# Kernel tuning notes

Hardware: AMD Instinct MI355X
Metric: run time of the kernel (lower is better)

## Reference

```python
import jax, jax.numpy as jnp
import numpy as np

LOW_THRESH, HIGH_THRESH = 0.1, 0.2   # kornia canny defaults
HYST_ITERS = 10                      # fixed-point hysteresis iterations (fixed for jit)


def _gaussian_kernel5(sigma=1.0):
    x = jnp.arange(5, dtype=jnp.float32) - 2.0
    g = jnp.exp(-0.5 * (x / sigma) ** 2)
    g = g / g.sum()
    return jnp.outer(g, g)  # [5,5]


def _conv2d(x, k):
    # x: [B,1,H,W]; k: [kh,kw]; reflect pad + VALID conv == SAME with reflect border
    kh, kw = k.shape
    xp = jnp.pad(x, ((0, 0), (0, 0), (kh // 2, kh // 2), (kw // 2, kw // 2)), mode="reflect")
    return jax.lax.conv_general_dilated(
        xp, k[None, None], (1, 1), "VALID",
        dimension_numbers=("NCHW", "OIHW", "NCHW"))


def _shift(x, dy, dx):
    # value of neighbor at (i+dy, j+dx), zero-padded border; x: [B,1,H,W]
    H, W = x.shape[2], x.shape[3]
    xp = jnp.pad(x, ((0, 0), (0, 0), (1, 1), (1, 1)))
    return xp[:, :, 1 + dy:1 + dy + H, 1 + dx:1 + dx + W]


def _canny_edges(img):
    # img: [B,3,H,W] in [0,1] -> binary edge map [B,1,H,W]
    gray = 0.299 * img[:, :1] + 0.587 * img[:, 1:2] + 0.114 * img[:, 2:3]
    blur = _conv2d(gray, _gaussian_kernel5())
    sobel_x = jnp.array([[-1., 0., 1.], [-2., 0., 2.], [-1., 0., 1.]], jnp.float32)
    gx = _conv2d(blur, sobel_x)
    gy = _conv2d(blur, sobel_x.T)
    mag = jnp.sqrt(gx * gx + gy * gy + 1e-12)
    ang = jnp.arctan2(gy, gx)

    # non-maximum suppression: quantize gradient direction to 4 bins (0/45/90/135 deg)
    b = jnp.mod(jnp.round(ang / (jnp.pi / 4.0)), 4).astype(jnp.int32)  # [B,1,H,W]
    n_pos = jnp.stack([_shift(mag, 0, 1), _shift(mag, 1, 1),
                       _shift(mag, 1, 0), _shift(mag, 1, -1)], axis=0)  # [4,B,1,H,W]
    n_neg = jnp.stack([_shift(mag, 0, -1), _shift(mag, -1, -1),
                       _shift(mag, -1, 0), _shift(mag, -1, 1)], axis=0)
    n1 = jnp.take_along_axis(n_pos, b[None], axis=0)[0]
    n2 = jnp.take_along_axis(n_neg, b[None], axis=0)[0]
    nms = jnp.where((mag >= n1) & (mag >= n2), mag, 0.0)

    # double threshold: strong=1.0, weak=0.5
    edges = jnp.where(nms >= HIGH_THRESH, 1.0,
                      jnp.where(nms >= LOW_THRESH, 0.5, 0.0))

    # hysteresis: weak pixels with a strong 8-neighbor become strong (iterated)
    def body(_, e):
        strong = (e == 1.0).astype(e.dtype)
        nb = jax.lax.reduce_window(strong, 0.0, jax.lax.max,
                                   (1, 1, 3, 3), (1, 1, 1, 1), "SAME")
        promoted = (e == 0.5) & (nb > 0.5)
        return jnp.where(promoted, 1.0, e)

    edges = jax.lax.fori_loop(0, HYST_ITERS, body, edges)
    return (edges == 1.0).astype(jnp.float32)


def setup_inputs() -> dict:
    key = jax.random.key(0)
    k1, k2 = jax.random.split(key)
    shape = (16, 3, 512, 512)
    return {"y_hat": jax.random.uniform(k1, shape, jnp.float32),
            "y": jax.random.uniform(k2, shape, jnp.float32)}


def reference(y_hat, y):
    y_hat_edges = _canny_edges(y_hat)
    y_edges = _canny_edges(y)
    return jnp.mean(jnp.abs(y_hat_edges - y_edges))  # F.l1_loss, mean reduction
```

## Files before the change

kernel.cpp:

```cpp
#include <hip/hip_runtime.h>
#include <math.h>

#define H 512
#define W 512
#define IMG (H*W)
#define NIMG 32

typedef unsigned long long u64;

__device__ __forceinline__ int reflect_idx(int i, int n) {
    if (i < 0) i = -i;
    if (i >= n) i = 2 * n - 2 - i;
    return i;
}

#define S0 0.05448868454964294f
#define S1 0.35317871110251920f
#define S2 0.94551131545035710f
#define S3 1.29364257779496160f
#define A1 0.05448868454964294f
#define A2 0.24420134200323332f
#define A3 0.34813126234460456f

#define TY 32

__global__ __launch_bounds__(512) void k_edges(const float* __restrict__ yhat,
                                               const float* __restrict__ yy,
                                               u64* __restrict__ strongP,
                                               u64* __restrict__ weakP) {
    __shared__ __align__(16) char lds[12768 + 22848];
    float (*sg)[76] = (float (*)[76])lds;
    float (*hxy)[68][2] = (float (*)[68][2])(lds + 12768);
    float (*sm)[68] = (float (*)[68])lds;
    unsigned char (*sbin)[68] = (unsigned char (*)[68])(lds + 9792);

    const int n = blockIdx.z;
    const float* src = (n < 16) ? (yhat + (size_t)n * 3 * IMG)
                                : (yy + (size_t)(n - 16) * 3 * IMG);
    const int x0 = blockIdx.x * 64;
    const int y0 = blockIdx.y * TY;
    const int tx = threadIdx.x, ty = threadIdx.y;
    const int tid = ty * 64 + tx;

    const int ixA = reflect_idx(x0 - 4 + tx, W);
    const int ixB = reflect_idx(x0 + 60 + tx, W);
#pragma unroll
    for (int k = 0; k < 6; k++) {
        int sy = ty + 8 * k;
        if (sy < 42) {
            int iy = reflect_idx(y0 - 4 + sy, H);
            const float* row = src + iy * W;
            float r = row[ixA], g = row[IMG + ixA], b = row[2 * IMG + ixA];
            sg[sy][tx] = 0.299f * r + 0.587f * g + 0.114f * b;
            if (tx < 8) {
                float r2 = row[ixB], g2 = row[IMG + ixB], b2 = row[2 * IMG + ixB];
                sg[sy][64 + tx] = 0.299f * r2 + 0.587f * g2 + 0.114f * b2;
            }
        }
    }
    __syncthreads();

    for (int t = tid; t < 714; t += 512) {
        int sy = t / 17, g = t % 17;
        const float4* p = (const float4*)&sg[sy][0];
        float4 q0 = p[g], q1 = p[g + 1], q2 = p[g + 2];
        float w[12] = {q0.x, q0.y, q0.z, q0.w, q1.x, q1.y, q1.z, q1.w,
                       q2.x, q2.y, q2.z, q2.w};
#pragma unroll
        for (int j = 0; j < 4; j++) {
            float hx = A3 * (w[j + 4] - w[j + 2]) + A2 * (w[j + 5] - w[j + 1])
                     + A1 * (w[j + 6] - w[j + 0]);
            float hy = S3 * w[j + 3] + S2 * (w[j + 4] + w[j + 2])
                     + S1 * (w[j + 5] + w[j + 1]) + S0 * (w[j + 6] + w[j + 0]);
            *(float2*)&hxy[sy][4 * g + j][0] = make_float2(hx, hy);
        }
    }
    __syncthreads();

    for (int t = tid; t < 594; t += 512) {
        int rg = t / 66, c = t % 66;
        float hx[10], hy[10];
#pragma unroll
        for (int i = 0; i < 10; i++) {
            float2 v = *(const float2*)&hxy[4 * rg + i][c][0];
            hx[i] = v.x; hy[i] = v.y;
        }
        int imgcol = x0 - 1 + c;
        bool colok = (unsigned)imgcol < (unsigned)W;
#pragma unroll
        for (int j = 0; j < 4; j++) {
            int my = 4 * rg + j;
            float gx = S3 * hx[j + 3] + S2 * (hx[j + 4] + hx[j + 2])
                     + S1 * (hx[j + 5] + hx[j + 1]) + S0 * (hx[j + 6] + hx[j + 0]);
            float gy = A3 * (hy[j + 4] - hy[j + 2]) + A2 * (hy[j + 5] - hy[j + 1])
                     + A1 * (hy[j + 6] - hy[j + 0]);
            int imgrow = y0 - 1 + my;
            bool ok = colok && ((unsigned)imgrow < (unsigned)H);
            float m = ok ? sqrtf(gx * gx + gy * gy + 1e-12f) : 0.f;
            sm[my][c] = m;
            float ax = fabsf(gx), ay = fabsf(gy);
            int d;
            if (ay <= 0.4142135623730951f * ax) d = 1;
            else if (ay >= 2.414213562373095f * ax) d = 68;
            else d = ((gx > 0.f) == (gy > 0.f)) ? 69 : 67;
            sbin[my][c] = (unsigned char)d;
        }
    }
    __syncthreads();

#pragma unroll
    for (int k = 0; k < 4; k++) {
        int ry = ty + 8 * k;
        const float* cp = &sm[ry + 1][tx + 1];
        float mag = cp[0];
        int d = sbin[ry + 1][tx + 1];
        float n1 = cp[d];
        float n2 = cp[-d];
        float nms = (mag >= n1 && mag >= n2) ? mag : 0.f;
        u64 strong = __ballot(nms >= 0.2f);
        u64 weak = __ballot(nms >= 0.1f);
        if (tx == 0) {
            size_t off = ((size_t)n * H + (y0 + ry)) * 8 + blockIdx.x;
            strongP[off] = strong;
            weakP[off] = weak;
        }
    }
}

__device__ __forceinline__ u64 ldw(const u64* p, int img, int y, int w, bool ok) {
    return (ok && w >= 0 && w < 8) ? p[((size_t)img * H + y) * 8 + w] : 0ULL;
}

__global__ __launch_bounds__(256) void k_hyst(const u64* __restrict__ strongP,
                                              const u64* __restrict__ weakP,
                                              unsigned int* __restrict__ partials) {
    __shared__ unsigned int part[4];
    const int wy = threadIdx.x >> 6;
    const int wave = blockIdx.x * 4 + wy;
    const int lane = threadIdx.x & 63;
    const int tile = wave & 255;
    const int pair = wave >> 8;
    const int tx0 = (tile & 15) * 32;
    const int ty0 = (tile >> 4) * 32;

    const int y = ty0 - 10 + lane;
    const bool rowok = (lane < 52) && (y >= 0) && (y < H);
    const int s = tx0 - 10;
    const int w0i = s >> 6;
    const int r = s & 63;

    const int imgA = pair, imgB = pair + 16;
    u64 sA, wA, sB, wB;
    {
        u64 lo, hi;
        lo = ldw(strongP, imgA, y, w0i, rowok); hi = ldw(strongP, imgA, y, w0i + 1, rowok);
        sA = (lo >> r) | (hi << (64 - r));
        lo = ldw(weakP, imgA, y, w0i, rowok);   hi = ldw(weakP, imgA, y, w0i + 1, rowok);
        wA = (lo >> r) | (hi << (64 - r));
        lo = ldw(strongP, imgB, y, w0i, rowok); hi = ldw(strongP, imgB, y, w0i + 1, rowok);
        sB = (lo >> r) | (hi << (64 - r));
        lo = ldw(weakP, imgB, y, w0i, rowok);   hi = ldw(weakP, imgB, y, w0i + 1, rowok);
        wB = (lo >> r) | (hi << (64 - r));
    }

#pragma unroll
    for (int it = 0; it < 10; it++) {
        u64 up = __shfl_up(sA, 1), dn = __shfl_down(sA, 1);
        u64 t = up | sA | dn;
        sA |= (t | (t << 1) | (t >> 1)) & wA;
        up = __shfl_up(sB, 1); dn = __shfl_down(sB, 1);
        t = up | sB | dn;
        sB |= (t | (t << 1) | (t >> 1)) & wB;
    }

    unsigned int c = 0;
    if (lane >= 10 && lane < 42) {
        const u64 mask = ((1ULL << 42) - (1ULL << 10));
        c = (unsigned int)__popcll((sA ^ sB) & mask);
    }
#pragma unroll
    for (int off = 32; off > 0; off >>= 1) c += __shfl_down(c, off);
    if (lane == 0) part[wy] = c;
    __syncthreads();
    if (threadIdx.x == 0)
        partials[blockIdx.x] = part[0] + part[1] + part[2] + part[3];
}

__global__ __launch_bounds__(256) void k_final(const unsigned int* __restrict__ partials,
                                               float* __restrict__ out) {
    __shared__ unsigned int part[4];
    unsigned int c = 0;
    for (int i = threadIdx.x; i < 1024; i += 256) c += partials[i];
#pragma unroll
    for (int off = 32; off > 0; off >>= 1) c += __shfl_down(c, off);
    const int lane = threadIdx.x & 63;
    const int wy = threadIdx.x >> 6;
    if (lane == 0) part[wy] = c;
    __syncthreads();
    if (threadIdx.x == 0)
        out[0] = (float)(part[0] + part[1] + part[2] + part[3]) * (1.0f / 4194304.0f);
}

extern "C" void kernel_launch(void* const* d_in, const int* in_sizes, int n_in,
                              void* d_out, int out_size, void* d_ws, size_t ws_size,
                              hipStream_t stream) {
    const float* yhat = (const float*)d_in[0];
    const float* yy = (const float*)d_in[1];

    u64* strongP = (u64*)d_ws;
    u64* weakP = strongP + (size_t)NIMG * H * 8;
    unsigned int* partials = (unsigned int*)(weakP + (size_t)NIMG * H * 8);

    dim3 eblk(64, 8);
    dim3 egrd(W / 64, H / TY, NIMG);
    k_edges<<<egrd, eblk, 0, stream>>>(yhat, yy, strongP, weakP);

    k_hyst<<<1024, 256, 0, stream>>>(strongP, weakP, partials);
    k_final<<<1, 256, 0, stream>>>(partials, (float*)d_out);
}
```

Before: 155.9 us.

## Vectorize gray tile loads with float4 and transpose bitplane layout for coalesced reads

Interior tiles now load the RGB halo with aligned float4 reads over an 80-wide shared-memory row that starts at x0-8. Border tiles fall back to a scalar reflect path. The strong and weak bitplanes are stored column-word-major (image, word, row), so the hysteresis kernel's per-lane row loads become contiguous. This is meant to cut global load instruction count and improve coalescing, at the cost of slightly more shared memory and a divergent border path.

```diff
diff --git a/kernel.cpp b/kernel.cpp
--- a/kernel.cpp
+++ b/kernel.cpp
@@ -28,9 +28,9 @@
                                                const float* __restrict__ yy,
                                                u64* __restrict__ strongP,
                                                u64* __restrict__ weakP) {
-    __shared__ __align__(16) char lds[12768 + 22848];
-    float (*sg)[76] = (float (*)[76])lds;
-    float (*hxy)[68][2] = (float (*)[68][2])(lds + 12768);
+    __shared__ __align__(16) char lds[13440 + 22848];
+    float (*sg)[80] = (float (*)[80])lds;
+    float (*hxy)[68][2] = (float (*)[68][2])(lds + 13440);
     float (*sm)[68] = (float (*)[68])lds;
     unsigned char (*sbin)[68] = (unsigned char (*)[68])(lds + 9792);
 
@@ -42,20 +42,29 @@
     const int tx = threadIdx.x, ty = threadIdx.y;
     const int tid = ty * 64 + tx;
 
-    const int ixA = reflect_idx(x0 - 4 + tx, W);
-    const int ixB = reflect_idx(x0 + 60 + tx, W);
-#pragma unroll
-    for (int k = 0; k < 6; k++) {
-        int sy = ty + 8 * k;
-        if (sy < 42) {
+    if (x0 >= 8 && x0 + 68 <= W) {
+        for (int t = tid; t < 42 * 19; t += 512) {
+            int sy = t / 19, f = t % 19;
             int iy = reflect_idx(y0 - 4 + sy, H);
-            const float* row = src + iy * W;
-            float r = row[ixA], g = row[IMG + ixA], b = row[2 * IMG + ixA];
-            sg[sy][tx] = 0.299f * r + 0.587f * g + 0.114f * b;
-            if (tx < 8) {
-                float r2 = row[ixB], g2 = row[IMG + ixB], b2 = row[2 * IMG + ixB];
-                sg[sy][64 + tx] = 0.299f * r2 + 0.587f * g2 + 0.114f * b2;
-            }
+            const float4* rp = (const float4*)(src + (size_t)iy * W + (x0 - 8));
+            float4 r = rp[f];
+            float4 g = rp[f + IMG / 4];
+            float4 b = rp[f + 2 * (IMG / 4)];
+            float4 gr;
+            gr.x = 0.299f * r.x + 0.587f * g.x + 0.114f * b.x;
+            gr.y = 0.299f * r.y + 0.587f * g.y + 0.114f * b.y;
+            gr.z = 0.299f * r.z + 0.587f * g.z + 0.114f * b.z;
+            gr.w = 0.299f * r.w + 0.587f * g.w + 0.114f * b.w;
+            *(float4*)&sg[sy][4 * f] = gr;
+        }
+    } else {
+        for (int t = tid; t < 42 * 76; t += 512) {
+            int sy = t / 76, c = t % 76;
+            int iy = reflect_idx(y0 - 4 + sy, H);
+            int ix = reflect_idx(x0 - 8 + c, W);
+            const float* row = src + (size_t)iy * W;
+            float r = row[ix], g = row[IMG + ix], b = row[2 * IMG + ix];
+            sg[sy][c] = 0.299f * r + 0.587f * g + 0.114f * b;
         }
     }
     __syncthreads();
@@ -63,7 +72,7 @@
     for (int t = tid; t < 714; t += 512) {
         int sy = t / 17, g = t % 17;
         const float4* p = (const float4*)&sg[sy][0];
-        float4 q0 = p[g], q1 = p[g + 1], q2 = p[g + 2];
+        float4 q0 = p[g + 1], q1 = p[g + 2], q2 = p[g + 3];
         float w[12] = {q0.x, q0.y, q0.z, q0.w, q1.x, q1.y, q1.z, q1.w,
                        q2.x, q2.y, q2.z, q2.w};
 #pragma unroll
@@ -120,7 +129,7 @@
         u64 strong = __ballot(nms >= 0.2f);
         u64 weak = __ballot(nms >= 0.1f);
         if (tx == 0) {
-            size_t off = ((size_t)n * H + (y0 + ry)) * 8 + blockIdx.x;
+            size_t off = ((size_t)n * 8 + blockIdx.x) * H + (y0 + ry);
             strongP[off] = strong;
             weakP[off] = weak;
         }
@@ -128,7 +137,7 @@
 }
 
 __device__ __forceinline__ u64 ldw(const u64* p, int img, int y, int w, bool ok) {
-    return (ok && w >= 0 && w < 8) ? p[((size_t)img * H + y) * 8 + w] : 0ULL;
+    return (ok && w >= 0 && w < 8) ? p[((size_t)img * 8 + w) * H + y] : 0ULL;
 }
 
 __global__ __launch_bounds__(256) void k_hyst(const u64* __restrict__ strongP,
@@ -145,6 +154,7 @@
 
     const int y = ty0 - 10 + lane;
     const bool rowok = (lane < 52) && (y >= 0) && (y < H);
+    const int yc = rowok ? y : 0;
     const int s = tx0 - 10;
     const int w0i = s >> 6;
     const int r = s & 63;
@@ -153,13 +163,13 @@
     u64 sA, wA, sB, wB;
     {
         u64 lo, hi;
-        lo = ldw(strongP, imgA, y, w0i, rowok); hi = ldw(strongP, imgA, y, w0i + 1, rowok);
+        lo = ldw(strongP, imgA, yc, w0i, rowok); hi = ldw(strongP, imgA, yc, w0i + 1, rowok);
         sA = (lo >> r) | (hi << (64 - r));
-        lo = ldw(weakP, imgA, y, w0i, rowok);   hi = ldw(weakP, imgA, y, w0i + 1, rowok);
+        lo = ldw(weakP, imgA, yc, w0i, rowok);   hi = ldw(weakP, imgA, yc, w0i + 1, rowok);
         wA = (lo >> r) | (hi << (64 - r));
-        lo = ldw(strongP, imgB, y, w0i, rowok); hi = ldw(strongP, imgB, y, w0i + 1, rowok);
+        lo = ldw(strongP, imgB, yc, w0i, rowok); hi = ldw(strongP, imgB, yc, w0i + 1, rowok);
         sB = (lo >> r) | (hi << (64 - r));
-        lo = ldw(weakP, imgB, y, w0i, rowok);   hi = ldw(weakP, imgB, y, w0i + 1, rowok);
+        lo = ldw(weakP, imgB, yc, w0i, rowok);   hi = ldw(weakP, imgB, yc, w0i + 1, rowok);
         wB = (lo >> r) | (hi << (64 - r));
     }
 
```

Result: faster. 142.8 us (-8.4%).
